# Kernel tuning notes

Measured on AMD Instinct MI355X. Metric: run time of the kernel, lower is better.

## Reference

```python
import jax, jax.numpy as jnp
import numpy as np
import math

B, S, D = 4, 2048, 1024
H = 16
HD = D // H  # 64
NEG_INF = -1e9


def setup_inputs() -> dict:
    key = jax.random.key(0)
    k1, k2, k3, k4, k5 = jax.random.split(key, 5)
    x = jax.random.normal(k1, (B, S, D), dtype=jnp.float32)
    # rotary frequencies (theta = 10000), shape (S, HD//2)
    inv_freq = 1.0 / (10000.0 ** (jnp.arange(0, HD, 2, dtype=jnp.float32) / HD))
    t = jnp.arange(S, dtype=jnp.float32)
    freqs = jnp.outer(t, inv_freq)  # (S, HD//2)
    freqs_cos = jnp.cos(freqs)
    freqs_sin = jnp.sin(freqs)
    # causal additive mask (1,1,S,S)
    causal = jnp.tril(jnp.ones((S, S), dtype=bool))
    mask = jnp.where(causal, 0.0, NEG_INF).astype(jnp.float32)[None, None]
    scale = 0.02
    wq = jax.random.normal(k2, (D, D), dtype=jnp.float32) * scale
    wk = jax.random.normal(k3, (D, D), dtype=jnp.float32) * scale
    wv = jax.random.normal(k4, (D, D), dtype=jnp.float32) * scale
    wo = jax.random.normal(k5, (D, D), dtype=jnp.float32) * scale
    return {"x": x, "freqs_cos": freqs_cos, "freqs_sin": freqs_sin,
            "mask": mask, "wq": wq, "wk": wk, "wv": wv, "wo": wo}


def _apply_rotary(t, cos, sin):
    # t: (B,S,H,HD); cos/sin: (S, HD//2) broadcast as (1,S,1,HD//2)
    tr = t.reshape(*t.shape[:-1], HD // 2, 2)
    t0, t1 = tr[..., 0], tr[..., 1]
    c = cos[None, :, None, :]
    s = sin[None, :, None, :]
    o0 = t0 * c - t1 * s
    o1 = t0 * s + t1 * c
    return jnp.stack([o0, o1], axis=-1).reshape(t.shape)


def reference(x, freqs_cos, freqs_sin, mask, wq, wk, wv, wo):
    bsz, seqlen, _ = x.shape
    xq = (x @ wq).reshape(bsz, seqlen, H, HD)
    xk = (x @ wk).reshape(bsz, seqlen, H, HD)
    xv = (x @ wv).reshape(bsz, seqlen, H, HD)
    xq = _apply_rotary(xq, freqs_cos, freqs_sin)
    xk = _apply_rotary(xk, freqs_cos, freqs_sin)
    # (B,H,S,HD)
    xq = xq.transpose(0, 2, 1, 3)
    xk = xk.transpose(0, 2, 1, 3)
    xv = xv.transpose(0, 2, 1, 3)
    scores = jnp.einsum('bhqd,bhkd->bhqk', xq, xk) / math.sqrt(HD)
    scores = scores + mask
    probs = jax.nn.softmax(scores.astype(jnp.float32), axis=-1).astype(xq.dtype)
    # dropout is identity in eval mode
    out = jnp.einsum('bhqk,bhkd->bhqd', probs, xv)
    out = out.transpose(0, 2, 1, 3).reshape(bsz, seqlen, H * HD)
    return out @ wo
```

## Files before the change

kernel.cpp:

```cpp
#include <hip/hip_runtime.h>
#include <stdint.h>

typedef short short8 __attribute__((ext_vector_type(8)));
typedef float f32x4 __attribute__((ext_vector_type(4)));
typedef float f32x16 __attribute__((ext_vector_type(16)));
typedef unsigned int u32x4 __attribute__((ext_vector_type(4)));
typedef float float4e __attribute__((ext_vector_type(4)));
typedef unsigned short u16;

#define BB 4
#define SS 2048
#define DD 1024
#define HH 16
#define MM (BB*SS)

__device__ __forceinline__ u16 f2bf(float f) {
    unsigned u = __float_as_uint(f);
    u += 0x7FFFu + ((u >> 16) & 1u);
    return (u16)(u >> 16);
}
__device__ __forceinline__ float bf2f(u16 h) {
    return __uint_as_float(((unsigned)h) << 16);
}
__device__ __forceinline__ unsigned cvtpk(float a, float b) {
    unsigned r;
    asm("v_cvt_pk_bf16_f32 %0, %1, %2" : "=v"(r) : "v"(a), "v"(b));
    return r;
}
__device__ __forceinline__ void gload16(const void* g, void* l) {
    __builtin_amdgcn_global_load_lds(
        (const __attribute__((address_space(1))) unsigned int*)(uintptr_t)g,
        (__attribute__((address_space(3))) unsigned int*)(unsigned)(uintptr_t)l,
        16, 0, 0);
}
__device__ __forceinline__ bool tens_is_bf(const u16* mref) { return mref[1] == 0xCE6Eu; }

__global__ __launch_bounds__(256) void cvt_x(const void* xin, u16* xb, const u16* mref) {
    bool isbf = tens_is_bf(mref);
    size_t i = (size_t)blockIdx.x * 256 + threadIdx.x;
    if (isbf) {
        ((u32x4*)xb)[i] = ((const u32x4*)xin)[i];
    } else {
        const float4e* src = (const float4e*)xin;
        float4e a = src[2*i], b = src[2*i+1];
        u32x4 o;
        o[0] = (unsigned)f2bf(a[0]) | ((unsigned)f2bf(a[1]) << 16);
        o[1] = (unsigned)f2bf(a[2]) | ((unsigned)f2bf(a[3]) << 16);
        o[2] = (unsigned)f2bf(b[0]) | ((unsigned)f2bf(b[1]) << 16);
        o[3] = (unsigned)f2bf(b[2]) | ((unsigned)f2bf(b[3]) << 16);
        ((u32x4*)xb)[i] = o;
    }
}

__global__ __launch_bounds__(256) void trw(const void* w0, const void* w1, const void* w2, const void* w3,
                                           u16* wt, const u16* mref) {
    bool isbf = tens_is_bf(mref);
    const void* w = (blockIdx.z == 0) ? w0 : (blockIdx.z == 1) ? w1 : (blockIdx.z == 2) ? w2 : w3;
    u16* out = wt + (size_t)blockIdx.z * (DD*DD);
    __shared__ float t[32][33];
    int tx = threadIdx.x & 31, ty = threadIdx.x >> 5;
    int n0 = blockIdx.x * 32, k0 = blockIdx.y * 32;
#pragma unroll
    for (int i = 0; i < 4; ++i) {
        int k = k0 + ty*4 + i;
        float v = isbf ? bf2f(((const u16*)w)[(size_t)k*DD + n0 + tx])
                       : ((const float*)w)[(size_t)k*DD + n0 + tx];
        t[ty*4 + i][tx] = v;
    }
    __syncthreads();
#pragma unroll
    for (int i = 0; i < 4; ++i)
        out[(size_t)(n0 + ty*4 + i)*DD + k0 + tx] = f2bf(t[tx][ty*4 + i]);
}

template<int MODE>
__global__ __launch_bounds__(256) void gemm128(const u16* __restrict__ A, const u16* __restrict__ Bt,
                                               void* Cout, const void* fcos, const void* fsin,
                                               const u16* mref, float oscale) {
    constexpr int SMEMB = (MODE == 2) ? 36864 : 32768;
    __shared__ __align__(16) unsigned char smem[SMEMB];
    int tid = threadIdx.x;
    int w = tid >> 6, l = tid & 63, lo = l & 15, hi = l >> 4;
    int wm = w >> 1, wn = w & 1;
    int m0 = blockIdx.x * 128, n0 = blockIdx.y * 128;

    f32x4 acc[4][4] = {};

    auto stage = [&](int buf, int t) {
        int k0 = t * 32;
#pragma unroll
        for (int i = 0; i < 2; ++i) {
            int o = (i*256 + tid) * 16;
            int row = o >> 6, inb = o & 63;
            int sw  = inb ^ ((row & 3) << 4);
            gload16((const char*)A + ((size_t)(m0 + row)*DD + k0)*2 + sw,
                    smem + buf*16384 + (i*256 + (tid & ~63))*16);
            gload16((const char*)Bt + ((size_t)(n0 + row)*DD + k0)*2 + sw,
                    smem + buf*16384 + 8192 + (i*256 + (tid & ~63))*16);
        }
    };

    stage(0, 0);
    __syncthreads();
    int cur = 0;
    const int NT = DD / 32;
    for (int t = 0; t < NT; ++t) {
        if (t + 1 < NT) stage(cur ^ 1, t + 1);
        const char* Ab = (const char*)(smem + cur*16384);
        const char* Bb = Ab + 8192;
        short8 af[4], bfr[4];
#pragma unroll
        for (int mi = 0; mi < 4; ++mi) {
            int r = wm*64 + mi*16 + lo;
            int ib = hi * 16;
            af[mi] = *(const short8*)(Ab + r*64 + (ib ^ ((r & 3) << 4)));
        }
#pragma unroll
        for (int ni = 0; ni < 4; ++ni) {
            int r = wn*64 + ni*16 + lo;
            int ib = hi * 16;
            bfr[ni] = *(const short8*)(Bb + r*64 + (ib ^ ((r & 3) << 4)));
        }
        __builtin_amdgcn_s_setprio(1);
#pragma unroll
        for (int mi = 0; mi < 4; ++mi)
#pragma unroll
            for (int ni = 0; ni < 4; ++ni)
                acc[mi][ni] = __builtin_amdgcn_mfma_f32_16x16x32_bf16(af[mi], bfr[ni], acc[mi][ni], 0, 0, 0);
        __builtin_amdgcn_s_setprio(0);
        __syncthreads();
        cur ^= 1;
    }

    if (MODE == 0) {
        bool fbf = (((const u16*)fcos)[0] == 0x3F80u);
        u16* outp = (u16*)Cout;
#pragma unroll
        for (int mi = 0; mi < 4; ++mi)
#pragma unroll
            for (int ni = 0; ni < 4; ++ni)
#pragma unroll
                for (int r = 0; r < 4; ++r) {
                    int gm = m0 + wm*64 + mi*16 + hi*4 + r;
                    int gc = n0 + wn*64 + ni*16 + lo;
                    float v  = acc[mi][ni][r];
                    float vp = __shfl_xor(v, 1);
                    int s = gm & (SS-1), d = gc & 63, i2 = d >> 1;
                    float c, sn;
                    if (fbf) { c = bf2f(((const u16*)fcos)[s*32 + i2]); sn = bf2f(((const u16*)fsin)[s*32 + i2]); }
                    else     { c = ((const float*)fcos)[s*32 + i2];     sn = ((const float*)fsin)[s*32 + i2]; }
                    float o = (gc & 1) ? (vp*sn + v*c) : (v*c - vp*sn);
                    o *= oscale;
                    int b = gm >> 11, h = gc >> 6;
                    outp[((((size_t)b*HH + h)*SS + s) << 6) + d] = f2bf(o);
                }
    } else if (MODE == 2) {
        __syncthreads();
        u16* vs = (u16*)smem + w * (64*72);
#pragma unroll
        for (int ni = 0; ni < 4; ++ni) {
            int d = ni*16 + lo;
#pragma unroll
            for (int mi = 0; mi < 4; ++mi)
#pragma unroll
                for (int rr = 0; rr < 2; ++rr) {
                    unsigned pk = (unsigned)f2bf(acc[mi][ni][2*rr]) | ((unsigned)f2bf(acc[mi][ni][2*rr+1]) << 16);
                    *(unsigned*)(vs + d*72 + mi*16 + hi*4 + rr*2) = pk;
                }
        }
        asm volatile("s_waitcnt lgkmcnt(0)" ::: "memory");
        int bq = (m0 + wm*64) >> 11;
        int s_base = (m0 + wm*64) & (SS-1);
        int h = (n0 + wn*64) >> 6;
        u16* outp = (u16*)Cout;
#pragma unroll
        for (int p = 0; p < 8; ++p) {
            int idx = p*64 + l;
            int row = idx >> 3, ch = idx & 7;
            short8 vv = *(const short8*)(vs + row*72 + ch*8);
            *(short8*)(outp + (((size_t)bq*HH + h)*64 + row)*SS + s_base + ch*8) = vv;
        }
    } else {
        bool isbf = tens_is_bf(mref);
#pragma unroll
        for (int mi = 0; mi < 4; ++mi)
#pragma unroll
            for (int ni = 0; ni < 4; ++ni)
#pragma unroll
                for (int r = 0; r < 4; ++r) {
                    int gm = m0 + wm*64 + mi*16 + hi*4 + r;
                    int gc = n0 + wn*64 + ni*16 + lo;
                    float v = acc[mi][ni][r];
                    if (isbf) ((u16*)Cout)[(size_t)gm*DD + gc] = f2bf(v);
                    else      ((float*)Cout)[(size_t)gm*DD + gc] = v;
                }
    }
}

__global__ __launch_bounds__(256) void attn(const u16* __restrict__ Q, const u16* __restrict__ K,
                                            const u16* __restrict__ VT, u16* __restrict__ AO) {
    __shared__ __align__(16) u16 Kl[2][64*64];
    __shared__ __align__(16) u16 Vl[2][64*64];
    int bh = blockIdx.x;
    int qt = (gridDim.y - 1) - blockIdx.y;
    int tid = threadIdx.x, w = tid >> 6, l = tid & 63;
    int l31 = l & 31, hi5 = l >> 5;
    const u16* Qb = Q  + (size_t)bh * SS * 64;
    const u16* Kb = K  + (size_t)bh * SS * 64;
    const u16* Vb = VT + (size_t)bh * 64 * SS;
    int q0w = qt*128 + w*32;
    int q   = q0w + l31;

    short8 qf[4];
#pragma unroll
    for (int kc = 0; kc < 4; ++kc)
        qf[kc] = *(const short8*)(Qb + (size_t)q*64 + kc*16 + hi5*8);

    f32x16 oacc[2] = {};
    float m_ = -1e30f, l_ = 0.f;

    auto stage = [&](int buf, int kt) {
        const char* Kt = (const char*)(Kb + (size_t)kt*64*64);
        const char* Vt = (const char*)Vb + (size_t)kt*128;
#pragma unroll
        for (int i = 0; i < 2; ++i) {
            int idx = i*256 + tid;
            int row = idx >> 3, inb = (idx & 7) * 16;
            int sw = inb ^ ((row & 7) << 4);
            gload16(Kt + row*128 + sw,            (char*)Kl[buf] + (i*256 + (tid & ~63))*16);
            gload16(Vt + (size_t)row*(SS*2) + sw, (char*)Vl[buf] + (i*256 + (tid & ~63))*16);
        }
    };

    int nkt = 2*qt + 2;
    stage(0, 0);
    __syncthreads();
    int cur = 0;

    for (int kt = 0; kt < nkt; ++kt) {
        if (kt + 1 < nkt) stage(cur ^ 1, kt + 1);

        if (kt*64 <= q0w + 31) {
            f32x16 sc[2] = {};
            __builtin_amdgcn_s_setprio(1);
#pragma unroll
            for (int kvt = 0; kvt < 2; ++kvt) {
                short8 kf[4];
#pragma unroll
                for (int kc = 0; kc < 4; ++kc) {
                    int row = kvt*32 + l31;
                    int ib = kc*32 + hi5*16;
                    kf[kc] = *(const short8*)((const char*)Kl[cur] + row*128 + (ib ^ ((row & 7) << 4)));
                }
#pragma unroll
                for (int kc = 0; kc < 4; ++kc)
                    sc[kvt] = __builtin_amdgcn_mfma_f32_32x32x16_bf16(kf[kc], qf[kc], sc[kvt], 0, 0, 0);
            }
            __builtin_amdgcn_s_setprio(0);

            if (kt*64 + 63 > q0w) {
#pragma unroll
                for (int kvt = 0; kvt < 2; ++kvt)
#pragma unroll
                    for (int rg = 0; rg < 16; ++rg) {
                        int kv = kt*64 + kvt*32 + (rg & 3) + 8*(rg >> 2) + 4*hi5;
                        if (kv > q) sc[kvt][rg] = -1e9f;
                    }
            }

            float mx = -1e30f;
#pragma unroll
            for (int kvt = 0; kvt < 2; ++kvt)
#pragma unroll
                for (int rg = 0; rg < 16; ++rg) mx = fmaxf(mx, sc[kvt][rg]);
            mx = fmaxf(mx, __shfl_xor(mx, 32));
            float mn = fmaxf(m_, mx);
            float al = __expf(m_ - mn);
            float rs = 0.f;
#pragma unroll
            for (int kvt = 0; kvt < 2; ++kvt)
#pragma unroll
                for (int rg = 0; rg < 16; ++rg) {
                    float p = __expf(sc[kvt][rg] - mn);
                    sc[kvt][rg] = p;
                    rs += p;
                }
            rs += __shfl_xor(rs, 32);
            m_ = mn;
            l_ = l_ * al + rs;
#pragma unroll
            for (int dt = 0; dt < 2; ++dt)
#pragma unroll
                for (int rg = 0; rg < 16; ++rg) oacc[dt][rg] *= al;

            short8 pa[4];
#pragma unroll
            for (int kc = 0; kc < 4; ++kc) {
                const int kvt = kc >> 1;
                const int base = (kc & 1) * 8;
                unsigned A0 = cvtpk(sc[kvt][base + 0], sc[kvt][base + 1]);
                unsigned A1 = cvtpk(sc[kvt][base + 2], sc[kvt][base + 3]);
                unsigned B0 = cvtpk(sc[kvt][base + 4], sc[kvt][base + 5]);
                unsigned B1 = cvtpk(sc[kvt][base + 6], sc[kvt][base + 7]);
                asm("v_permlane32_swap_b32 %0, %1" : "+v"(A0), "+v"(B0));
                asm("v_permlane32_swap_b32 %0, %1" : "+v"(A1), "+v"(B1));
                u32x4 pk; pk[0] = A0; pk[1] = A1; pk[2] = B0; pk[3] = B1;
                pa[kc] = __builtin_bit_cast(short8, pk);
            }

            __builtin_amdgcn_s_setprio(1);
#pragma unroll
            for (int dt = 0; dt < 2; ++dt) {
                short8 vf[4];
#pragma unroll
                for (int kc = 0; kc < 4; ++kc) {
                    int row = dt*32 + l31;
                    int ib = kc*32 + hi5*16;
                    vf[kc] = *(const short8*)((const char*)Vl[cur] + row*128 + (ib ^ ((row & 7) << 4)));
                }
#pragma unroll
                for (int kc = 0; kc < 4; ++kc)
                    oacc[dt] = __builtin_amdgcn_mfma_f32_32x32x16_bf16(vf[kc], pa[kc], oacc[dt], 0, 0, 0);
            }
            __builtin_amdgcn_s_setprio(0);
        }

        __syncthreads();
        cur ^= 1;
    }

    int b = bh >> 4, h = bh & 15;
    float inv = 1.0f / l_;
    u16* aor = AO + (size_t)(b*SS + q)*DD + h*64;
#pragma unroll
    for (int dt = 0; dt < 2; ++dt)
#pragma unroll
        for (int j = 0; j < 8; ++j) {
            int r0 = 2*j, r1 = 2*j + 1;
            int d = dt*32 + (r0 & 3) + 8*(r0 >> 2) + 4*hi5;
            unsigned pk = (unsigned)f2bf(oacc[dt][r0] * inv) | ((unsigned)f2bf(oacc[dt][r1] * inv) << 16);
            *(unsigned*)(aor + d) = pk;
        }
}

extern "C" void kernel_launch(void* const* d_in, const int* in_sizes, int n_in,
                              void* d_out, int out_size, void* d_ws, size_t ws_size,
                              hipStream_t stream) {
    const void* x    = d_in[0];
    const void* fcos = d_in[1];
    const void* fsin = d_in[2];
    const u16*  mref = (const u16*)d_in[3];
    const void* wq   = d_in[4];
    const void* wk   = d_in[5];
    const void* wv   = d_in[6];
    const void* wo   = d_in[7];

    u16* ws = (u16*)d_ws;
    const size_t XB = (size_t)MM * DD;
    const size_t WT = (size_t)DD * DD;
    u16* xb  = ws;
    u16* wt  = ws + XB;
    u16* qb  = ws + XB + 4*WT;
    u16* kb  = qb + XB;
    u16* vtb = kb + XB;

    cvt_x<<<4096, 256, 0, stream>>>(x, xb, mref);
    trw<<<dim3(32, 32, 4), 256, 0, stream>>>(wq, wk, wv, wo, wt, mref);
    gemm128<0><<<dim3(64, 8), 256, 0, stream>>>(xb, wt,        qb,  fcos, fsin, mref, 0.125f);
    gemm128<0><<<dim3(64, 8), 256, 0, stream>>>(xb, wt + WT,   kb,  fcos, fsin, mref, 1.0f);
    gemm128<2><<<dim3(64, 8), 256, 0, stream>>>(xb, wt + 2*WT, vtb, fcos, fsin, mref, 1.0f);
    attn<<<dim3(64, 16), 256, 0, stream>>>(qb, kb, vtb, xb);
    gemm128<3><<<dim3(64, 8), 256, 0, stream>>>(xb, wt + 3*WT, d_out, fcos, fsin, mref, 1.0f);
}
```

Baseline: 194.8 us.

## Merge Q/K/V projections into one launch and shrink GEMM N-tile to 64

Replaces the three separate Q, K and V projection launches with a single launch that picks the weight by blockIdx.z, with each block's epilogue doing rotary, scaling or the V transpose. The GEMM tile shrinks from 128x128 to 128x64, which doubles the block count (1536 for QKV, 1024 for the output projection) and cuts shared memory to 24 KB. The goal is better CU occupancy and fewer launch gaps and tail effects on the 256-CU device. The cost is lower per-block data reuse, since more A-tile reloads from global/L2 are needed per unit of output.

New measurement: 200.6 us. +3.0%, slower.

```diff
diff --git a/kernel.cpp b/kernel.cpp
--- a/kernel.cpp
+++ b/kernel.cpp
@@ -74,29 +74,35 @@
 }
 
 template<int MODE>
-__global__ __launch_bounds__(256) void gemm128(const u16* __restrict__ A, const u16* __restrict__ Bt,
-                                               void* Cout, const void* fcos, const void* fsin,
-                                               const u16* mref, float oscale) {
-    constexpr int SMEMB = (MODE == 2) ? 36864 : 32768;
-    __shared__ __align__(16) unsigned char smem[SMEMB];
+__global__ __launch_bounds__(256) void gemm64(const u16* __restrict__ A, const u16* __restrict__ wt,
+                                              u16* outQ, u16* outK, u16* outVT, void* Cout,
+                                              const void* fcos, const void* fsin,
+                                              const u16* mref) {
+    __shared__ __align__(16) unsigned char smem[24576];
     int tid = threadIdx.x;
     int w = tid >> 6, l = tid & 63, lo = l & 15, hi = l >> 4;
     int wm = w >> 1, wn = w & 1;
-    int m0 = blockIdx.x * 128, n0 = blockIdx.y * 128;
-
-    f32x4 acc[4][4] = {};
+    int m0 = blockIdx.x * 128, n0 = blockIdx.y * 64;
+    int wi = (MODE == 1) ? (int)blockIdx.z : 3;
+    const u16* Bt = (MODE == 1) ? wt + (size_t)wi * (DD*DD) : wt;
+
+    f32x4 acc[4][2] = {};
 
     auto stage = [&](int buf, int t) {
         int k0 = t * 32;
 #pragma unroll
         for (int i = 0; i < 2; ++i) {
-            int o = (i*256 + tid) * 16;
-            int row = o >> 6, inb = o & 63;
+            int idx = i*256 + tid;
+            int row = idx >> 2, inb = (idx & 3) * 16;
             int sw  = inb ^ ((row & 3) << 4);
             gload16((const char*)A + ((size_t)(m0 + row)*DD + k0)*2 + sw,
-                    smem + buf*16384 + (i*256 + (tid & ~63))*16);
+                    smem + buf*12288 + (i*256 + (tid & ~63))*16);
+        }
+        {
+            int row = tid >> 2, inb = (tid & 3) * 16;
+            int sw  = inb ^ ((row & 3) << 4);
             gload16((const char*)Bt + ((size_t)(n0 + row)*DD + k0)*2 + sw,
-                    smem + buf*16384 + 8192 + (i*256 + (tid & ~63))*16);
+                    smem + buf*12288 + 8192 + (tid & ~63)*16);
         }
     };
 
@@ -106,43 +112,69 @@
     const int NT = DD / 32;
     for (int t = 0; t < NT; ++t) {
         if (t + 1 < NT) stage(cur ^ 1, t + 1);
-        const char* Ab = (const char*)(smem + cur*16384);
+        const char* Ab = (const char*)(smem + cur*12288);
         const char* Bb = Ab + 8192;
-        short8 af[4], bfr[4];
+        short8 af[4], bfr[2];
 #pragma unroll
         for (int mi = 0; mi < 4; ++mi) {
             int r = wm*64 + mi*16 + lo;
-            int ib = hi * 16;
-            af[mi] = *(const short8*)(Ab + r*64 + (ib ^ ((r & 3) << 4)));
-        }
-#pragma unroll
-        for (int ni = 0; ni < 4; ++ni) {
-            int r = wn*64 + ni*16 + lo;
-            int ib = hi * 16;
-            bfr[ni] = *(const short8*)(Bb + r*64 + (ib ^ ((r & 3) << 4)));
+            af[mi] = *(const short8*)(Ab + r*64 + ((hi*16) ^ ((r & 3) << 4)));
+        }
+#pragma unroll
+        for (int ni = 0; ni < 2; ++ni) {
+            int r = wn*32 + ni*16 + lo;
+            bfr[ni] = *(const short8*)(Bb + r*64 + ((hi*16) ^ ((r & 3) << 4)));
         }
         __builtin_amdgcn_s_setprio(1);
 #pragma unroll
         for (int mi = 0; mi < 4; ++mi)
 #pragma unroll
-            for (int ni = 0; ni < 4; ++ni)
+            for (int ni = 0; ni < 2; ++ni)
                 acc[mi][ni] = __builtin_amdgcn_mfma_f32_16x16x32_bf16(af[mi], bfr[ni], acc[mi][ni], 0, 0, 0);
         __builtin_amdgcn_s_setprio(0);
         __syncthreads();
         cur ^= 1;
     }
 
-    if (MODE == 0) {
+    if (MODE == 1 && wi == 2) {
+        __syncthreads();
+        u16* vs = (u16*)smem + w * (32*72);
+#pragma unroll
+        for (int ni = 0; ni < 2; ++ni) {
+            int d = ni*16 + lo;
+#pragma unroll
+            for (int mi = 0; mi < 4; ++mi)
+#pragma unroll
+                for (int rr = 0; rr < 2; ++rr) {
+                    unsigned pk = (unsigned)f2bf(acc[mi][ni][2*rr]) | ((unsigned)f2bf(acc[mi][ni][2*rr+1]) << 16);
+                    *(unsigned*)(vs + d*72 + mi*16 + hi*4 + rr*2) = pk;
+                }
+        }
+        asm volatile("s_waitcnt lgkmcnt(0)" ::: "memory");
+        int srow0 = m0 + wm*64;
+        int bq = srow0 >> 11;
+        int s_base = srow0 & (SS-1);
+        int h = n0 >> 6;
+#pragma unroll
+        for (int p = 0; p < 4; ++p) {
+            int idx = p*64 + l;
+            int row = idx >> 3, ch = idx & 7;
+            short8 vv = *(const short8*)(vs + row*72 + ch*8);
+            int d = wn*32 + row;
+            *(short8*)(outVT + (((size_t)bq*HH + h)*64 + d)*SS + s_base + ch*8) = vv;
+        }
+    } else if (MODE == 1) {
         bool fbf = (((const u16*)fcos)[0] == 0x3F80u);
-        u16* outp = (u16*)Cout;
+        u16* outp = wi ? outK : outQ;
+        float oscale = wi ? 1.0f : 0.125f;
 #pragma unroll
         for (int mi = 0; mi < 4; ++mi)
 #pragma unroll
-            for (int ni = 0; ni < 4; ++ni)
+            for (int ni = 0; ni < 2; ++ni)
 #pragma unroll
                 for (int r = 0; r < 4; ++r) {
                     int gm = m0 + wm*64 + mi*16 + hi*4 + r;
-                    int gc = n0 + wn*64 + ni*16 + lo;
+                    int gc = n0 + wn*32 + ni*16 + lo;
                     float v  = acc[mi][ni][r];
                     float vp = __shfl_xor(v, 1);
                     int s = gm & (SS-1), d = gc & 63, i2 = d >> 1;
@@ -154,42 +186,16 @@
                     int b = gm >> 11, h = gc >> 6;
                     outp[((((size_t)b*HH + h)*SS + s) << 6) + d] = f2bf(o);
                 }
-    } else if (MODE == 2) {
-        __syncthreads();
-        u16* vs = (u16*)smem + w * (64*72);
-#pragma unroll
-        for (int ni = 0; ni < 4; ++ni) {
-            int d = ni*16 + lo;
-#pragma unroll
-            for (int mi = 0; mi < 4; ++mi)
-#pragma unroll
-                for (int rr = 0; rr < 2; ++rr) {
-                    unsigned pk = (unsigned)f2bf(acc[mi][ni][2*rr]) | ((unsigned)f2bf(acc[mi][ni][2*rr+1]) << 16);
-                    *(unsigned*)(vs + d*72 + mi*16 + hi*4 + rr*2) = pk;
-                }
-        }
-        asm volatile("s_waitcnt lgkmcnt(0)" ::: "memory");
-        int bq = (m0 + wm*64) >> 11;
-        int s_base = (m0 + wm*64) & (SS-1);
-        int h = (n0 + wn*64) >> 6;
-        u16* outp = (u16*)Cout;
-#pragma unroll
-        for (int p = 0; p < 8; ++p) {
-            int idx = p*64 + l;
-            int row = idx >> 3, ch = idx & 7;
-            short8 vv = *(const short8*)(vs + row*72 + ch*8);
-            *(short8*)(outp + (((size_t)bq*HH + h)*64 + row)*SS + s_base + ch*8) = vv;
-        }
     } else {
         bool isbf = tens_is_bf(mref);
 #pragma unroll
         for (int mi = 0; mi < 4; ++mi)
 #pragma unroll
-            for (int ni = 0; ni < 4; ++ni)
+            for (int ni = 0; ni < 2; ++ni)
 #pragma unroll
                 for (int r = 0; r < 4; ++r) {
                     int gm = m0 + wm*64 + mi*16 + hi*4 + r;
-                    int gc = n0 + wn*64 + ni*16 + lo;
+                    int gc = n0 + wn*32 + ni*16 + lo;
                     float v = acc[mi][ni][r];
                     if (isbf) ((u16*)Cout)[(size_t)gm*DD + gc] = f2bf(v);
                     else      ((float*)Cout)[(size_t)gm*DD + gc] = v;
@@ -366,9 +372,7 @@
 
     cvt_x<<<4096, 256, 0, stream>>>(x, xb, mref);
     trw<<<dim3(32, 32, 4), 256, 0, stream>>>(wq, wk, wv, wo, wt, mref);
-    gemm128<0><<<dim3(64, 8), 256, 0, stream>>>(xb, wt,        qb,  fcos, fsin, mref, 0.125f);
-    gemm128<0><<<dim3(64, 8), 256, 0, stream>>>(xb, wt + WT,   kb,  fcos, fsin, mref, 1.0f);
-    gemm128<2><<<dim3(64, 8), 256, 0, stream>>>(xb, wt + 2*WT, vtb, fcos, fsin, mref, 1.0f);
+    gemm64<1><<<dim3(64, 16, 3), 256, 0, stream>>>(xb, wt, qb, kb, vtb, nullptr, fcos, fsin, mref);
     attn<<<dim3(64, 16), 256, 0, stream>>>(qb, kb, vtb, xb);
-    gemm128<3><<<dim3(64, 8), 256, 0, stream>>>(xb, wt + 3*WT, d_out, fcos, fsin, mref, 1.0f);
-}
+    gemm64<3><<<dim3(64, 16), 256, 0, stream>>>(xb, wt + 3*WT, nullptr, nullptr, nullptr, d_out, fcos, fsin, mref);
+}
```
